# Optimization experiments

Measured on AMD Instinct MI355X. Metric: run time of the kernel, lower is better.

Reference implementation:

```python
import jax, jax.numpy as jnp
import numpy as np

N = 10000      # nodes
E = 160000     # edges (avg degree 16)
R = 4          # num_relations
H = 3          # heads
B = 100        # graphs in the batch
ED = 8         # edge_dim
NEG = 0.2      # leaky_relu negative slope (PyG default)

CONVS = [(768, 128), (256, 384), (256, 128), (256, 128)]  # (in, out) per RGATConv
LINS = [(128, 256), (384, 256), (128, 256), (128, 256)]


def setup_inputs() -> dict:
    key = jax.random.key(0)
    ks = iter(jax.random.split(key, 64))
    p = lambda shape: jax.random.normal(next(ks), shape, dtype=jnp.float32) * 0.05
    inp = {
        "x": jax.random.normal(next(ks), (N, 768), dtype=jnp.float32),
        "edge_index": jax.random.randint(next(ks), (2, E), 0, N),
        "edge_type": jax.random.randint(next(ks), (E,), 0, R),
        "edge_attr": jax.random.normal(next(ks), (E, ED), dtype=jnp.float32),
        "batch": jnp.repeat(jnp.arange(B, dtype=jnp.int32), N // B),  # sorted graph ids
    }
    for i, (cin, cout) in enumerate(CONVS, 1):
        ho = H * cout
        inp[f"W{i}"] = p((R, cin, ho))
        inp[f"q{i}"] = p((ho, H))
        inp[f"k{i}"] = p((ho, H))
        inp[f"le{i}"] = p((ED, ho))
        inp[f"e{i}"] = p((ho, H))
        inp[f"b{i}"] = jnp.zeros((cout,), jnp.float32)
    for i, (cin, cout) in enumerate(LINS, 1):
        inp[f"lw{i}"] = p((cin, cout))
        inp[f"lb{i}"] = jnp.zeros((cout,), jnp.float32)
    return inp


def _segment_softmax(a, index, n):
    # softmax of per-edge scores a (E, H) over destination-node segments
    amax = jax.ops.segment_max(a, index, num_segments=n)
    amax = jnp.where(jnp.isfinite(amax), amax, 0.0)
    ex = jnp.exp(a - amax[index])
    s = jax.ops.segment_sum(ex, index, num_segments=n)
    return ex / jnp.maximum(s[index], 1e-16)


def _rgat(x, src, dst, etype, eattr, W, q, k, le, e, b, cout):
    n = x.shape[0]
    xW = jnp.einsum('ni,rio->nro', x, W)           # (N, R, H*O): per-relation transform
    qn = jnp.einsum('nro,oh->nrh', xW, q)          # node-level query scores
    kn = jnp.einsum('nro,oh->nrh', xW, k)          # node-level key scores
    qi = qn[dst, etype]                            # (E, H)
    kj = kn[src, etype]                            # (E, H)
    ae = (eattr @ le) @ e                          # (E, H) edge-feature scores
    alpha = jax.nn.leaky_relu(qi + kj + ae, NEG)
    alpha = _segment_softmax(alpha, dst, n)        # across-relation segment softmax
    outj = xW[src, etype].reshape(-1, H, cout)     # (E, H, O)
    msg = alpha[:, :, None] * outj
    aggr = jax.ops.segment_sum(msg, dst, num_segments=n)  # (N, H, O)
    return aggr.mean(axis=1) + b                   # concat=False -> mean over heads


def reference(x, edge_index, edge_type, edge_attr, batch,
              W1, q1, k1, le1, e1, b1, W2, q2, k2, le2, e2, b2,
              W3, q3, k3, le3, e3, b3, W4, q4, k4, le4, e4, b4,
              lw1, lb1, lw2, lb2, lw3, lb3, lw4, lb4):
    src, dst = edge_index[0], edge_index[1]
    convs = [(W1, q1, k1, le1, e1, b1), (W2, q2, k2, le2, e2, b2),
             (W3, q3, k3, le3, e3, b3), (W4, q4, k4, le4, e4, b4)]
    lins = [(lw1, lb1), (lw2, lb2), (lw3, lb3), (lw4, lb4)]
    h = x
    for (W, q, k, le, e, b), (lw, lb), (cin, cout) in zip(convs, lins, CONVS):
        h = _rgat(h, src, dst, edge_type, edge_attr, W, q, k, le, e, b, cout)
        h = h @ lw + lb
    # dropout is identity in eval; pick first node of each graph (hole node)
    hole_idx = jax.ops.segment_min(jnp.arange(h.shape[0]), batch, num_segments=B)
    return jax.nn.softmax(h[hole_idx], axis=1)     # (B, 256)
```

## Files before the change

### kernel.cpp

```cpp
#include <hip/hip_runtime.h>

typedef unsigned int uint;
typedef unsigned short ushort;
typedef __attribute__((ext_vector_type(8))) short bf16x8;
typedef __attribute__((ext_vector_type(4))) float f32x4;

#define GLD_LDS(g, l) __builtin_amdgcn_global_load_lds( \
    (const __attribute__((address_space(1))) void*)(g), \
    (__attribute__((address_space(3))) void*)(l), 16, 0, 0)

__device__ __forceinline__ ushort f2bf(float f) {
    uint u = __builtin_bit_cast(uint, f);
    u += 0x7fffu + ((u >> 16) & 1u);
    return (ushort)(u >> 16);
}
__device__ __forceinline__ float bf2f(ushort s) {
    uint u = ((uint)s) << 16;
    return __builtin_bit_cast(float, u);
}
__device__ __forceinline__ void wave_sync() {
    asm volatile("s_waitcnt lgkmcnt(0)" ::: "memory");
}
__device__ __forceinline__ float wave_max(float v) {
#pragma unroll
    for (int d = 32; d >= 1; d >>= 1) v = fmaxf(v, __shfl_xor(v, d));
    return v;
}
__device__ __forceinline__ float wave_sum(float v) {
#pragma unroll
    for (int d = 32; d >= 1; d >>= 1) v += __shfl_xor(v, d);
    return v;
}

__global__ void deg_hole_kernel(const int* __restrict__ dst, int* __restrict__ cnt,
                                const int* __restrict__ bat, int* __restrict__ hole,
                                int E, int N) {
    int e = blockIdx.x * 256 + threadIdx.x;
    if (e < E) atomicAdd(&cnt[dst[e]], 1);
    if (e < N) atomicMin(&hole[bat[e]], e);
}

__global__ void scan_kernel(const int* __restrict__ cnt, int* __restrict__ offs, int n) {
    __shared__ int part[1024];
    const int t = threadIdx.x;
    const int strip = (n + 1023) / 1024;
    int s = 0;
    for (int i = 0; i < strip; ++i) {
        int idx = t * strip + i;
        if (idx < n) s += cnt[idx];
    }
    part[t] = s;
    __syncthreads();
    for (int d = 1; d < 1024; d <<= 1) {
        int v = (t >= d) ? part[t - d] : 0;
        __syncthreads();
        part[t] += v;
        __syncthreads();
    }
    int run = (t == 0) ? 0 : part[t - 1];
    for (int i = 0; i < strip; ++i) {
        int idx = t * strip + i;
        if (idx < n) { offs[idx] = run; run += cnt[idx]; }
    }
    if (t == 1023) offs[n] = part[1023];
}

__global__ void fill_kernel(const int* __restrict__ dst, const int* __restrict__ offs,
                            int* __restrict__ cur, int* __restrict__ csr, int E) {
    int e = blockIdx.x * 256 + threadIdx.x;
    if (e < E) {
        int d = dst[e];
        int p = offs[d] + atomicAdd(&cur[d], 1);
        csr[p] = e;
    }
}

struct PrepSArgs {
    const float *W0, *W1, *W2, *W3, *q0, *q1, *q2, *q3, *k0, *k1, *k2, *k3;
    float *Wqk0, *Wqk1, *Wqk2, *Wqk3;
    const float *le0, *le1, *le2, *le3, *e0, *e1, *e2, *e3;
    float* g;
    const float *b2, *lw2l, *lb2;
    float* bf2;
};

__device__ __forceinline__ void wqk_body(const float* W, const float* q, const float* k,
                                         float* Wqk, int cin, int ho, int i, int lane) {
    int c = i >> 2, r = i & 3;
    const float* wrow = W + ((long)r * cin + c) * ho;
    float sq0 = 0.f, sq1 = 0.f, sq2 = 0.f, sk0 = 0.f, sk1 = 0.f, sk2 = 0.f;
    for (int o = lane; o < ho; o += 64) {
        float w = wrow[o];
        sq0 += w * q[(long)o * 3 + 0];
        sq1 += w * q[(long)o * 3 + 1];
        sq2 += w * q[(long)o * 3 + 2];
        sk0 += w * k[(long)o * 3 + 0];
        sk1 += w * k[(long)o * 3 + 1];
        sk2 += w * k[(long)o * 3 + 2];
    }
    sq0 = wave_sum(sq0); sq1 = wave_sum(sq1); sq2 = wave_sum(sq2);
    sk0 = wave_sum(sk0); sk1 = wave_sum(sk1); sk2 = wave_sum(sk2);
    if (lane == 0) {
        float* w6 = Wqk + (long)c * 24 + r * 6;
        w6[0] = sq0; w6[1] = sq1; w6[2] = sq2;
        w6[3] = sk0; w6[4] = sk1; w6[5] = sk2;
    }
}

__global__ __launch_bounds__(256)
void preps_kernel(PrepSArgs a) {
    const int wid = threadIdx.x >> 6, lane = threadIdx.x & 63;
    int w = blockIdx.x * 4 + wid;
    if (w < 96) {
        int l = w / 24, j = w % 24;
        int d = j / 3, h = j % 3;
        const float* le = (l == 0) ? a.le0 : (l == 1 ? a.le1 : (l == 2 ? a.le2 : a.le3));
        const float* e  = (l == 0) ? a.e0  : (l == 1 ? a.e1  : (l == 2 ? a.e2  : a.e3));
        int ho = (l == 1) ? 1152 : 384;
        float s = 0.f;
        for (int o = lane; o < ho; o += 64) s += le[(long)d * ho + o] * e[(long)o * 3 + h];
        s = wave_sum(s);
        if (lane == 0) a.g[l * 24 + j] = s;
        return;
    }
    w -= 96;
    if (w < 3072) { wqk_body(a.W0, a.q0, a.k0, a.Wqk0, 768, 384, w, lane); return; }
    w -= 3072;
    if (w < 1024) { wqk_body(a.W1, a.q1, a.k1, a.Wqk1, 256, 1152, w, lane); return; }
    w -= 1024;
    if (w < 1024) { wqk_body(a.W2, a.q2, a.k2, a.Wqk2, 256, 384, w, lane); return; }
    w -= 1024;
    if (w < 1024) { wqk_body(a.W3, a.q3, a.k3, a.Wqk3, 256, 384, w, lane); return; }
    w -= 1024;
    if (w < 256) {
        float s = 0.f;
        for (int o = lane; o < 384; o += 64) s += a.b2[o] * a.lw2l[(long)o * 256 + w];
        s = wave_sum(s);
        if (lane == 0) a.bf2[w] = s + a.lb2[w];
    }
}

struct PrepWArgs {
    const float *x, *W0, *W2, *W3, *lw0, *lw1, *lw2, *lw3, *W1;
    ushort *hbf, *Wt0, *Wt2, *Wt3, *lwT0, *lwT1, *lwT2, *lwT3, *A2;
    const float* Wqk0;
};

__device__ __forceinline__ void trW_body(const float* W, ushort* Wt, int cin, int ho, long idx) {
    long ncol = idx / cin;
    int c = (int)(idx % cin);
    int r = (int)(ncol / ho);
    int o = (int)(ncol % ho);
    Wt[idx] = f2bf(W[((long)r * cin + c) * ho + o]);
}
__device__ __forceinline__ void trLw_body(const float* lw, ushort* lwT, int cout_in, long idx) {
    int o = (int)(idx / cout_in);
    int c = (int)(idx % cout_in);
    lwT[idx] = f2bf(lw[(long)c * 256 + o]);
}

__global__ __launch_bounds__(256)
void prepw_kernel(PrepWArgs a, int nbCast, long nCast) {
    int b = blockIdx.x;
    const int t = threadIdx.x;
    if (b < nbCast) {
        long i = ((long)b * 256 + t) * 4;
        if (i + 4 <= nCast) {
            float4 v = *(const float4*)(a.x + i);
            ushort4 o4 = { f2bf(v.x), f2bf(v.y), f2bf(v.z), f2bf(v.w) };
            *(ushort4*)(a.hbf + i) = o4;
        }
        return;
    }
    b -= nbCast;
    if (b < 4608) { trW_body(a.W0, a.Wt0, 768, 384, (long)b * 256 + t); return; }
    b -= 4608;
    if (b < 1536) { trW_body(a.W2, a.Wt2, 256, 384, (long)b * 256 + t); return; }
    b -= 1536;
    if (b < 1536) { trW_body(a.W3, a.Wt3, 256, 384, (long)b * 256 + t); return; }
    b -= 1536;
    if (b < 128)  { trLw_body(a.lw0, a.lwT0, 128, (long)b * 256 + t); return; }
    b -= 128;
    if (b < 384)  { trLw_body(a.lw1, a.lwT1, 384, (long)b * 256 + t); return; }
    b -= 384;
    if (b < 128)  { trLw_body(a.lw2, a.lwT2, 128, (long)b * 256 + t); return; }
    b -= 128;
    if (b < 128)  { trLw_body(a.lw3, a.lwT3, 128, (long)b * 256 + t); return; }
    b -= 128;
    if (b < 1728) {
        long idx = (long)b * 256 + t;
        int j = (int)(idx / 384), o = (int)(idx % 384);
        int h = j >> 10, rc = j & 1023;
        int r = rc >> 8, c = rc & 255;
        a.A2[idx] = f2bf(a.W1[((long)(r * 256 + c)) * 1152 + h * 384 + o] * (1.f / 3.f));
        return;
    }
    b -= 1728;
    if (b < 72) {
        long idx = (long)b * 256 + t;
        int j = (int)(idx / 768), c = (int)(idx % 768);
        a.Wt0[(long)(1536 + j) * 768 + c] = f2bf(a.Wqk0[(long)c * 24 + j]);
        return;
    }
    b -= 72;
    a.Wt0[(long)1560 * 768 + (long)b * 256 + t] = 0;
}

__global__ __launch_bounds__(256)
void prep2_kernel(const float* __restrict__ ea, const float* __restrict__ g,
                  float* __restrict__ aeb, int E, int nbAe,
                  const float* __restrict__ lw0, const float* __restrict__ Wqk1,
                  const float* __restrict__ lb0, ushort* __restrict__ lwT0, float* __restrict__ qb1,
                  const float* __restrict__ lw2, const float* __restrict__ Wqk3,
                  const float* __restrict__ lb2, ushort* __restrict__ lwT2, float* __restrict__ qb3) {
    int b = blockIdx.x;
    const int t = threadIdx.x;
    if (b < nbAe) {
        int e = b * 256 + t;
        if (e >= E) return;
        float a[8];
#pragma unroll
        for (int d = 0; d < 8; ++d) a[d] = ea[(long)e * 8 + d];
#pragma unroll
        for (int l = 0; l < 4; ++l) {
#pragma unroll
            for (int h = 0; h < 3; ++h) {
                float s = 0.f;
#pragma unroll
                for (int d = 0; d < 8; ++d) s += a[d] * g[l * 24 + d * 3 + h];
                aeb[((size_t)l * E + e) * 3 + h] = s;
            }
        }
        return;
    }
    b -= nbAe;
    const int wid = t >> 6, lane = t & 63;
    if (b < 768) {
        int w = b * 4 + wid;
        int c = w / 24, j = w % 24;
        float s = 0.f;
        for (int o = lane; o < 256; o += 64) s += lw0[(long)c * 256 + o] * Wqk1[(long)o * 24 + j];
        s = wave_sum(s);
        if (lane == 0) lwT0[(256 + j) * 128 + c] = f2bf(s);
        return;
    }
    b -= 768;
    if (b < 768) {
        int w = b * 4 + wid;
        int c = w / 24, j = w % 24;
        float s = 0.f;
        for (int o = lane; o < 256; o += 64) s += lw2[(long)c * 256 + o] * Wqk3[(long)o * 24 + j];
        s = wave_sum(s);
        if (lane == 0) lwT2[(256 + j) * 128 + c] = f2bf(s);
        return;
    }
    b -= 768;
    if (b < 6) {
        int w = b * 4 + wid;
        if (w < 24) {
            float s = 0.f;
            for (int o = lane; o < 256; o += 64) s += lb0[o] * Wqk1[(long)o * 24 + w];
            s = wave_sum(s);
            if (lane == 0) qb1[w] = s;
        }
        return;
    }
    b -= 6;
    if (b < 6) {
        int w = b * 4 + wid;
        if (w < 24) {
            float s = 0.f;
            for (int o = lane; o < 256; o += 64) s += lb2[o] * Wqk3[(long)o * 24 + w];
            s = wave_sum(s);
            if (lane == 0) qb3[w] = s;
        }
        return;
    }
    b -= 6;
    if (b < 52) { lwT0[280 * 128 + b * 256 + t] = 0; return; }
    b -= 52;
    lwT2[280 * 128 + b * 256 + t] = 0;
}

template<int OUT_BF16, int DUAL, int PARTIAL, int QK>
__global__ __launch_bounds__(256, 5)
void gemm_bf16(const ushort* __restrict__ A, const ushort* __restrict__ Bt,
               void* __restrict__ Cp, ushort* __restrict__ C2,
               const float* __restrict__ bias,
               int M, int K, int ldc, int nbn, int nwg, int nbase, int Ks,
               float* __restrict__ qkn, const float* __restrict__ qb, int qkcol) {
    __shared__ ushort lA[2][128 * 32];
    __shared__ ushort lB[2][128 * 32];
    const int t = threadIdx.x;
    const int lane = t & 63;
    const int wid = t >> 6;

    int b = blockIdx.x;
    int q8 = nwg >> 3, r8 = nwg & 7;
    int xcd = b & 7, loc = b >> 3;
    int tt = (xcd < r8 ? xcd * (q8 + 1) : r8 * (q8 + 1) + (xcd - r8) * q8) + loc;
    const int slice = tt / nbase;
    const int tile = tt % nbase;
    const int kbase = slice * Ks;
    const int bm = (tile / nbn) * 128;
    const int bn = (tile % nbn) * 128;

    const int wr = (wid >> 1) * 64;
    const int wc = (wid & 1) * 64;

    f32x4 acc[4][4];
#pragma unroll
    for (int m = 0; m < 4; ++m)
#pragma unroll
        for (int nn = 0; nn < 4; ++nn) acc[m][nn] = (f32x4){0.f, 0.f, 0.f, 0.f};

    const int sr = t >> 2;
    const int sk = (((t & 3) ^ ((t >> 3) & 3)) * 8);
    long ar0 = bm + sr;      if (ar0 > M - 1) ar0 = M - 1;
    long ar1 = bm + sr + 64; if (ar1 > M - 1) ar1 = M - 1;
    const ushort* gA0 = A + ar0 * K + sk + kbase;
    const ushort* gA1 = A + ar1 * K + sk + kbase;
    const ushort* gB0 = Bt + (long)(bn + sr) * K + sk + kbase;
    const ushort* gB1 = Bt + (long)(bn + sr + 64) * K + sk + kbase;

    const int frow = lane & 15;
    const int pc8 = (((lane >> 4) ^ ((lane >> 1) & 3)) * 8);

    GLD_LDS(gA0, &lA[0][t * 8]);
    GLD_LDS(gA1, &lA[0][t * 8 + 64 * 32]);
    GLD_LDS(gB0, &lB[0][t * 8]);
    GLD_LDS(gB1, &lB[0][t * 8 + 64 * 32]);
    __syncthreads();

    int cur = 0;
    for (int k0 = 0; k0 < Ks; k0 += 32) {
        if (k0 + 32 < Ks) {
            int nb = cur ^ 1, kn = k0 + 32;
            GLD_LDS(gA0 + kn, &lA[nb][t * 8]);
            GLD_LDS(gA1 + kn, &lA[nb][t * 8 + 64 * 32]);
            GLD_LDS(gB0 + kn, &lB[nb][t * 8]);
            GLD_LDS(gB1 + kn, &lB[nb][t * 8 + 64 * 32]);
        }
        bf16x8 af[4], bff[4];
#pragma unroll
        for (int m = 0; m < 4; ++m)
            af[m] = *(const bf16x8*)&lA[cur][(wr + m * 16 + frow) * 32 + pc8];
#pragma unroll
        for (int nn = 0; nn < 4; ++nn)
            bff[nn] = *(const bf16x8*)&lB[cur][(wc + nn * 16 + frow) * 32 + pc8];
#pragma unroll
        for (int m = 0; m < 4; ++m)
#pragma unroll
            for (int nn = 0; nn < 4; ++nn)
                acc[m][nn] = __builtin_amdgcn_mfma_f32_16x16x32_bf16(af[m], bff[nn], acc[m][nn], 0, 0, 0);
        __syncthreads();
        cur ^= 1;
    }

    const int crow = (lane >> 4) * 4;
    const int ccol = lane & 15;
#pragma unroll
    for (int m = 0; m < 4; ++m) {
#pragma unroll
        for (int nn = 0; nn < 4; ++nn) {
            int col = bn + wc + nn * 16 + ccol;
#pragma unroll
            for (int r = 0; r < 4; ++r) {
                int row = bm + wr + m * 16 + crow + r;
                if (row < M) {
                    float v = acc[m][nn][r];
                    if (QK && col >= qkcol) {
                        int qc = col - qkcol;
                        if (qc < 24) qkn[(long)row * 24 + qc] = v + (qb ? qb[qc] : 0.f);
                    } else {
                        if (!PARTIAL && bias) v += bias[col];
                        if (PARTIAL) {
                            ((float*)Cp)[(size_t)slice * M * ldc + (long)row * ldc + col] = v;
                        } else {
                            if (OUT_BF16) ((ushort*)Cp)[(long)row * ldc + col] = f2bf(v);
                            else          ((float*)Cp)[(long)row * ldc + col] = v;
                            if (DUAL)     C2[(long)row * ldc + col] = f2bf(v);
                        }
                    }
                }
            }
        }
    }
}

__global__ __launch_bounds__(256)
void reduce3qk_kernel(const float* __restrict__ P, const float* __restrict__ bf2,
                      const float* __restrict__ Wqk2,
                      float* __restrict__ outf, ushort* __restrict__ outb,
                      float* __restrict__ qkn, int M) {
    const int wid = threadIdx.x >> 6, lane = threadIdx.x & 63;
    const int n = blockIdx.x * 4 + wid;
    if (n >= M) return;
    long off = (long)n * 256 + lane * 4;
    const long stride = (long)M * 256;
    float4 a = *(const float4*)(P + off);
    float4 b = *(const float4*)(P + stride + off);
    float4 c = *(const float4*)(P + 2 * stride + off);
    float4 bs = *(const float4*)(bf2 + lane * 4);
    float rr[4] = { a.x + b.x + c.x + bs.x, a.y + b.y + c.y + bs.y,
                    a.z + b.z + c.z + bs.z, a.w + b.w + c.w + bs.w };
    float4 r4 = { rr[0], rr[1], rr[2], rr[3] };
    *(float4*)(outf + off) = r4;
    ushort4 o4 = { f2bf(rr[0]), f2bf(rr[1]), f2bf(rr[2]), f2bf(rr[3]) };
    *(ushort4*)(outb + off) = o4;
    float acc[24];
#pragma unroll
    for (int j = 0; j < 24; ++j) acc[j] = 0.f;
#pragma unroll
    for (int i = 0; i < 4; ++i) {
        const float* wr = Wqk2 + (long)(lane * 4 + i) * 24;
        float hv = rr[i];
#pragma unroll
        for (int j = 0; j < 24; ++j) acc[j] += hv * wr[j];
    }
#pragma unroll
    for (int j = 0; j < 24; ++j) {
        float v = wave_sum(acc[j]);
        if (lane == 0) qkn[(long)n * 24 + j] = v;
    }
}

__global__ __launch_bounds__(256)
void attn_kernel(const float* __restrict__ qkn, const ushort* __restrict__ xW,
                 const float* __restrict__ ae, const int* __restrict__ offs,
                 const int* __restrict__ csr, const int* __restrict__ srcv,
                 const int* __restrict__ etv, const float* __restrict__ bias,
                 ushort* __restrict__ out, int N) {
    __shared__ float4 pk_sh[4][64];
    __shared__ float red[4][384];
    const int wid = threadIdx.x >> 6, lane = threadIdx.x & 63;
    const int n = blockIdx.x * 4 + wid;
    if (n >= N) return;
    const int e0 = offs[n];
    const int deg = offs[n + 1] - e0;
    const float* qd = qkn + (long)n * 24;

    float m0 = -1e30f, m1 = -1e30f, m2 = -1e30f;
    for (int base = 0; base < deg; base += 64) {
        int idx = base + lane;
        if (idx < deg) {
            int eid = csr[e0 + idx];
            int s_ = srcv[eid], t_ = etv[eid];
            const float* qs = qkn + (long)s_ * 24 + t_ * 6;
            const float* a3 = ae + (long)eid * 3;
            float v0 = qd[t_ * 6 + 0] + qs[3] + a3[0];
            float v1 = qd[t_ * 6 + 1] + qs[4] + a3[1];
            float v2 = qd[t_ * 6 + 2] + qs[5] + a3[2];
            v0 = v0 > 0.f ? v0 : 0.2f * v0;
            v1 = v1 > 0.f ? v1 : 0.2f * v1;
            v2 = v2 > 0.f ? v2 : 0.2f * v2;
            m0 = fmaxf(m0, v0); m1 = fmaxf(m1, v1); m2 = fmaxf(m2, v2);
        }
    }
    m0 = wave_max(m0); m1 = wave_max(m1); m2 = wave_max(m2);

    float acc[6] = {0.f, 0.f, 0.f, 0.f, 0.f, 0.f};
    float ps0 = 0.f, ps1 = 0.f, ps2 = 0.f;

    for (int base = 0; base < deg; base += 64) {
        int cnt2 = deg - base; if (cnt2 > 64) cnt2 = 64;
        if (lane < cnt2) {
            int eid = csr[e0 + base + lane];
            int s_ = srcv[eid], t_ = etv[eid];
            const float* qs = qkn + (long)s_ * 24 + t_ * 6;
            const float* a3 = ae + (long)eid * 3;
            float v0 = qd[t_ * 6 + 0] + qs[3] + a3[0];
            float v1 = qd[t_ * 6 + 1] + qs[4] + a3[1];
            float v2 = qd[t_ * 6 + 2] + qs[5] + a3[2];
            v0 = v0 > 0.f ? v0 : 0.2f * v0;
            v1 = v1 > 0.f ? v1 : 0.2f * v1;
            v2 = v2 > 0.f ? v2 : 0.2f * v2;
            float p0 = __expf(v0 - m0), p1 = __expf(v1 - m1), p2 = __expf(v2 - m2);
            pk_sh[wid][lane] = make_float4(p0, p1, p2, __int_as_float((s_ << 2) | t_));
            ps0 += p0; ps1 += p1; ps2 += p2;
        }
        wave_sync();
        float4 pk0 = {0,0,0,0}, pk1 = {0,0,0,0}, pk2 = {0,0,0,0}, pk3 = {0,0,0,0};
        uint a0 = 0, b0 = 0, c0 = 0, a1 = 0, b1 = 0, c1 = 0;
        uint a2 = 0, b2 = 0, c2 = 0, a3 = 0, b3 = 0, c3 = 0;
#define LDE(S, J) { pk##S = pk_sh[wid][J]; \
    const uint* xr = (const uint*)(xW + (long)__float_as_int(pk##S.w) * 384); \
    a##S = xr[lane]; b##S = xr[lane + 64]; c##S = xr[lane + 128]; }
#define ACCE(S) { \
    acc[0] += pk##S.x * bf2f((ushort)(a##S & 0xffffu)); \
    acc[1] += pk##S.x * bf2f((ushort)(a##S >> 16)); \
    acc[2] += pk##S.y * bf2f((ushort)(b##S & 0xffffu)); \
    acc[3] += pk##S.y * bf2f((ushort)(b##S >> 16)); \
    acc[4] += pk##S.z * bf2f((ushort)(c##S & 0xffffu)); \
    acc[5] += pk##S.z * bf2f((ushort)(c##S >> 16)); }
        if (0 < cnt2) LDE(0, 0);
        if (1 < cnt2) LDE(1, 1);
        if (2 < cnt2) LDE(2, 2);
        if (3 < cnt2) LDE(3, 3);
        for (int j = 0; j < cnt2; j += 4) {
            { ACCE(0); if (j + 4 < cnt2) LDE(0, j + 4); }
            if (j + 1 < cnt2) { ACCE(1); if (j + 5 < cnt2) LDE(1, j + 5); }
            if (j + 2 < cnt2) { ACCE(2); if (j + 6 < cnt2) LDE(2, j + 6); }
            if (j + 3 < cnt2) { ACCE(3); if (j + 7 < cnt2) LDE(3, j + 7); }
        }
#undef LDE
#undef ACCE
        wave_sync();
    }
    ps0 = wave_sum(ps0); ps1 = wave_sum(ps1); ps2 = wave_sum(ps2);
    float i0 = 1.f / fmaxf(ps0, 1e-16f);
    float i1 = 1.f / fmaxf(ps1, 1e-16f);
    float i2 = 1.f / fmaxf(ps2, 1e-16f);
    red[wid][2 * lane]           = acc[0] * i0;
    red[wid][2 * lane + 1]       = acc[1] * i0;
    red[wid][128 + 2 * lane]     = acc[2] * i1;
    red[wid][128 + 2 * lane + 1] = acc[3] * i1;
    red[wid][256 + 2 * lane]     = acc[4] * i2;
    red[wid][256 + 2 * lane + 1] = acc[5] * i2;
    wave_sync();
    for (int o = lane; o < 128; o += 64) {
        float v = (red[wid][o] + red[wid][128 + o] + red[wid][256 + o]) * (1.f / 3.f) + bias[o];
        out[(long)n * 128 + o] = f2bf(v);
    }
}

__global__ __launch_bounds__(256)
void attn2_kernel(const float* __restrict__ qkn, const ushort* __restrict__ hbf,
                  const float* __restrict__ ae, const int* __restrict__ offs,
                  const int* __restrict__ csr, const int* __restrict__ srcv,
                  const int* __restrict__ etv, ushort* __restrict__ Z, int N) {
    __shared__ float4 pk_sh[4][64];
    const int wid = threadIdx.x >> 6, lane = threadIdx.x & 63;
    const int n = blockIdx.x * 4 + wid;
    if (n >= N) return;
    const int e0 = offs[n];
    const int deg = offs[n + 1] - e0;
    const float* qd = qkn + (long)n * 24;

    float m0 = -1e30f, m1 = -1e30f, m2 = -1e30f;
    for (int base = 0; base < deg; base += 64) {
        int idx = base + lane;
        if (idx < deg) {
            int eid = csr[e0 + idx];
            int s_ = srcv[eid], t_ = etv[eid];
            const float* qs = qkn + (long)s_ * 24 + t_ * 6;
            const float* a3 = ae + (long)eid * 3;
            float v0 = qd[t_ * 6 + 0] + qs[3] + a3[0];
            float v1 = qd[t_ * 6 + 1] + qs[4] + a3[1];
            float v2 = qd[t_ * 6 + 2] + qs[5] + a3[2];
            v0 = v0 > 0.f ? v0 : 0.2f * v0;
            v1 = v1 > 0.f ? v1 : 0.2f * v1;
            v2 = v2 > 0.f ? v2 : 0.2f * v2;
            m0 = fmaxf(m0, v0); m1 = fmaxf(m1, v1); m2 = fmaxf(m2, v2);
        }
    }
    m0 = wave_max(m0); m1 = wave_max(m1); m2 = wave_max(m2);

    float acc[48];
#pragma unroll
    for (int i = 0; i < 48; ++i) acc[i] = 0.f;
    float ps0 = 0.f, ps1 = 0.f, ps2 = 0.f;

    for (int base = 0; base < deg; base += 64) {
        int cnt2 = deg - base; if (cnt2 > 64) cnt2 = 64;
        if (lane < cnt2) {
            int eid = csr[e0 + base + lane];
            int s_ = srcv[eid], t_ = etv[eid];
            const float* qs = qkn + (long)s_ * 24 + t_ * 6;
            const float* a3 = ae + (long)eid * 3;
            float v0 = qd[t_ * 6 + 0] + qs[3] + a3[0];
            float v1 = qd[t_ * 6 + 1] + qs[4] + a3[1];
            float v2 = qd[t_ * 6 + 2] + qs[5] + a3[2];
            v0 = v0 > 0.f ? v0 : 0.2f * v0;
            v1 = v1 > 0.f ? v1 : 0.2f * v1;
            v2 = v2 > 0.f ? v2 : 0.2f * v2;
            float p0 = __expf(v0 - m0), p1 = __expf(v1 - m1), p2 = __expf(v2 - m2);
            pk_sh[wid][lane] = make_float4(p0, p1, p2, __int_as_float((s_ << 2) | t_));
            ps0 += p0; ps1 += p1; ps2 += p2;
        }
        wave_sync();
        float4 pk0 = {0,0,0,0}, pk1 = {0,0,0,0}, pk2 = {0,0,0,0}, pk3 = {0,0,0,0};
        uint2 v0_ = {0,0}, v1_ = {0,0}, v2_ = {0,0}, v3_ = {0,0};
#define LDE2(S, J) { pk##S = pk_sh[wid][J]; \
    v##S##_ = *(const uint2*)(hbf + ((long)(__float_as_int(pk##S.w) >> 2)) * 256 + lane * 4); }
#define UPDR(R) { \
    acc[(R)*4+0] += px * x0; acc[(R)*4+1] += px * x1; acc[(R)*4+2] += px * x2; acc[(R)*4+3] += px * x3; \
    acc[16+(R)*4+0] += py * x0; acc[16+(R)*4+1] += py * x1; acc[16+(R)*4+2] += py * x2; acc[16+(R)*4+3] += py * x3; \
    acc[32+(R)*4+0] += pz * x0; acc[32+(R)*4+1] += pz * x1; acc[32+(R)*4+2] += pz * x2; acc[32+(R)*4+3] += pz * x3; }
#define ACC2(S) { int r_ = __float_as_int(pk##S.w) & 3; \
    float x0 = bf2f((ushort)(v##S##_.x & 0xffffu)), x1 = bf2f((ushort)(v##S##_.x >> 16)); \
    float x2 = bf2f((ushort)(v##S##_.y & 0xffffu)), x3 = bf2f((ushort)(v##S##_.y >> 16)); \
    float px = pk##S.x, py = pk##S.y, pz = pk##S.z; \
    if (r_ == 0) UPDR(0) else if (r_ == 1) UPDR(1) else if (r_ == 2) UPDR(2) else UPDR(3) }
        if (0 < cnt2) LDE2(0, 0);
        if (1 < cnt2) LDE2(1, 1);
        if (2 < cnt2) LDE2(2, 2);
        if (3 < cnt2) LDE2(3, 3);
        for (int j = 0; j < cnt2; j += 4) {
            { ACC2(0); if (j + 4 < cnt2) LDE2(0, j + 4); }
            if (j + 1 < cnt2) { ACC2(1); if (j + 5 < cnt2) LDE2(1, j + 5); }
            if (j + 2 < cnt2) { ACC2(2); if (j + 6 < cnt2) LDE2(2, j + 6); }
            if (j + 3 < cnt2) { ACC2(3); if (j + 7 < cnt2) LDE2(3, j + 7); }
        }
#undef LDE2
#undef UPDR
#undef ACC2
        wave_sync();
    }
    ps0 = wave_sum(ps0); ps1 = wave_sum(ps1); ps2 = wave_sum(ps2);
    float inv0 = 1.f / fmaxf(ps0, 1e-16f);
    float inv1 = 1.f / fmaxf(ps1, 1e-16f);
    float inv2 = 1.f / fmaxf(ps2, 1e-16f);
    ushort* zr = Z + (long)n * 3072 + lane * 4;
#pragma unroll
    for (int h = 0; h < 3; ++h) {
        float iv = (h == 0) ? inv0 : (h == 1 ? inv1 : inv2);
#pragma unroll
        for (int r = 0; r < 4; ++r) {
            const float* a4 = acc + h * 16 + r * 4;
            ushort4 o4 = { f2bf(a4[0] * iv), f2bf(a4[1] * iv),
                           f2bf(a4[2] * iv), f2bf(a4[3] * iv) };
            *(ushort4*)(zr + h * 1024 + r * 256) = o4;
        }
    }
}

__global__ void softmax_kernel(const float* __restrict__ h, const int* __restrict__ hole,
                               float* __restrict__ out, int B) {
    int b = blockIdx.x;
    int t = threadIdx.x;
    int lane = t & 63, wid = t >> 6;
    __shared__ float sm[4];
    __shared__ float ss[4];
    int row = hole[b];
    float v = h[(long)row * 256 + t];
    float m = v;
#pragma unroll
    for (int d = 32; d >= 1; d >>= 1) m = fmaxf(m, __shfl_xor(m, d));
    if (lane == 0) sm[wid] = m;
    __syncthreads();
    m = fmaxf(fmaxf(sm[0], sm[1]), fmaxf(sm[2], sm[3]));
    float ex = __expf(v - m);
    float s = ex;
#pragma unroll
    for (int d = 32; d >= 1; d >>= 1) s += __shfl_xor(s, d);
    if (lane == 0) ss[wid] = s;
    __syncthreads();
    s = ss[0] + ss[1] + ss[2] + ss[3];
    out[(long)b * 256 + t] = ex / s;
}

extern "C" void kernel_launch(void* const* d_in, const int* in_sizes, int n_in,
                              void* d_out, int out_size, void* d_ws, size_t ws_size,
                              hipStream_t stream) {
    const float* x   = (const float*)d_in[0];
    const int*   ei  = (const int*)d_in[1];
    const int*   ety = (const int*)d_in[2];
    const float* ea  = (const float*)d_in[3];
    const int*   bat = (const int*)d_in[4];

    const int N = in_sizes[0] / 768;
    const int E = in_sizes[2];
    const int B = out_size / 256;

    static const int CIN[4]  = {768, 256, 256, 256};
    static const int COUT[4] = {128, 384, 128, 128};
    static const int NCC[4]  = {1536, 4608, 1536, 1536};

    const float *Wp[4], *qp[4], *kp[4], *lep[4], *ep[4], *bp[4], *lwp[4], *lbp[4];
    for (int l = 0; l < 4; ++l) {
        Wp[l]  = (const float*)d_in[5 + 6 * l];
        qp[l]  = (const float*)d_in[6 + 6 * l];
        kp[l]  = (const float*)d_in[7 + 6 * l];
        lep[l] = (const float*)d_in[8 + 6 * l];
        ep[l]  = (const float*)d_in[9 + 6 * l];
        bp[l]  = (const float*)d_in[10 + 6 * l];
        lwp[l] = (const float*)d_in[29 + 2 * l];
        lbp[l] = (const float*)d_in[30 + 2 * l];
    }

    char* ws = (char*)d_ws;
    size_t pos = 0;
    auto carve = [&](size_t bytes) -> char* {
        char* r = ws + pos;
        pos += (bytes + 255) & ~(size_t)255;
        return r;
    };
    ushort *Wt[4], *lwT[4];
    float* Wqk[4];
    for (int l = 0; l < 4; ++l) {
        size_t cols = (l == 0) ? 1664 : (size_t)NCC[l];
        Wt[l] = (ushort*)carve(l == 1 ? 0 : (size_t)2 * cols * CIN[l]);
    }
    for (int l = 0; l < 4; ++l) lwT[l] = (ushort*)carve((size_t)2 * 384 * COUT[l]);
    for (int l = 0; l < 4; ++l) Wqk[l] = (float*)carve((size_t)4 * 24 * CIN[l]);
    float*  gbuf  = (float*)carve(4 * 24 * 4);
    float*  aeb   = (float*)carve((size_t)4 * E * 3 * 4);
    float*  qkn   = (float*)carve((size_t)N * 24 * 4);
    float*  qb1   = (float*)carve(24 * 4);
    float*  qb3   = (float*)carve(24 * 4);
    ushort* hbf   = (ushort*)carve((size_t)N * 768 * 2);
    ushort* xWb   = (ushort*)carve((size_t)N * 1536 * 2);
    ushort* Zb    = (ushort*)carve((size_t)N * 3072 * 2);
    ushort* A2    = (ushort*)carve((size_t)3072 * 384 * 2);
    ushort* W2T   = (ushort*)carve((size_t)256 * 3072 * 2);
    float*  bf2   = (float*)carve(256 * 4);
    ushort* convbf= (ushort*)carve((size_t)N * 384 * 2);
    float*  hbuf  = (float*)carve((size_t)N * 256 * 4);
    int* cnt  = (int*)carve((size_t)N * 4);
    int* cur  = (int*)carve((size_t)N * 4);
    int* offs = (int*)carve((size_t)(N + 1) * 4);
    int* csr  = (int*)carve((size_t)E * 4);
    int* hole = (int*)carve((size_t)B * 4);

    hipMemsetAsync(cnt, 0, (size_t)((char*)cur - (char*)cnt) + (size_t)N * 4, stream);
    hipMemsetAsync(hole, 0x7f, (size_t)B * 4, stream);

    const int* dst = ei + E;
    int nbEH = ((E > N ? E : N) + 255) / 256;
    deg_hole_kernel<<<nbEH, 256, 0, stream>>>(dst, cnt, bat, hole, E, N);
    scan_kernel<<<1, 1024, 0, stream>>>(cnt, offs, N);
    fill_kernel<<<(E + 255) / 256, 256, 0, stream>>>(dst, offs, cur, csr, E);

    PrepSArgs psa = { Wp[0], Wp[1], Wp[2], Wp[3], qp[0], qp[1], qp[2], qp[3],
                      kp[0], kp[1], kp[2], kp[3], Wqk[0], Wqk[1], Wqk[2], Wqk[3],
                      lep[0], lep[1], lep[2], lep[3], ep[0], ep[1], ep[2], ep[3],
                      gbuf, bp[1], lwp[1], lbp[1], bf2 };
    preps_kernel<<<(6496 + 3) / 4, 256, 0, stream>>>(psa);

    long nCast = (long)N * 768;
    int nbCast = (int)((nCast / 4 + 255) / 256);
    PrepWArgs pw = { x, Wp[0], Wp[2], Wp[3], lwp[0], lwp[1], lwp[2], lwp[3], Wp[1],
                     hbf, Wt[0], Wt[2], Wt[3], lwT[0], lwT[1], lwT[2], lwT[3], A2, Wqk[0] };
    prepw_kernel<<<nbCast + 13056 + 72 + 312, 256, 0, stream>>>(pw, nbCast, nCast);

    int nbAe = (E + 255) / 256;
    prep2_kernel<<<nbAe + 1652, 256, 0, stream>>>(ea, gbuf, aeb, E, nbAe,
                                                  lwp[0], Wqk[1], lbp[0], lwT[0], qb1,
                                                  lwp[2], Wqk[3], lbp[2], lwT[2], qb3);

    gemm_bf16<1, 0, 0, 0><<<48, 256, 0, stream>>>(lwT[1], A2, (void*)W2T, nullptr, nullptr,
                                                  256, 384, 3072, 24, 48, 48, 384,
                                                  nullptr, nullptr, 0);

    const int nbm = (N + 127) / 128;
    for (int l = 0; l < 4; ++l) {
        if (l == 1) {
            attn2_kernel<<<(N + 3) / 4, 256, 0, stream>>>(qkn, hbf, aeb + (size_t)l * E * 3,
                                                          offs, csr, ei, ety, Zb, N);
            int nbase = nbm * 2, nwgS = nbase * 3;
            gemm_bf16<0, 0, 1, 0><<<nwgS, 256, 0, stream>>>(Zb, W2T, (void*)xWb, nullptr, nullptr,
                                                            N, 3072, 256, 2, nwgS, nbase, 1024,
                                                            nullptr, nullptr, 0);
            reduce3qk_kernel<<<(N + 3) / 4, 256, 0, stream>>>((const float*)xWb, bf2, Wqk[2],
                                                              hbuf, hbf, qkn, N);
        } else {
            if (l == 0) {
                int nbn1 = 13, nwg1 = nbm * nbn1;
                gemm_bf16<1, 0, 0, 1><<<nwg1, 256, 0, stream>>>(hbf, Wt[0], (void*)xWb, nullptr,
                                                                nullptr, N, 768, 1536, nbn1, nwg1,
                                                                nwg1, 768, qkn, nullptr, 1536);
            } else {
                int nbn1 = NCC[l] / 128, nwg1 = nbm * nbn1;
                gemm_bf16<1, 0, 0, 0><<<nwg1, 256, 0, stream>>>(hbf, Wt[l], (void*)xWb, nullptr,
                                                                nullptr, N, CIN[l], NCC[l], nbn1,
                                                                nwg1, nwg1, CIN[l],
                                                                nullptr, nullptr, 0);
            }
            attn_kernel<<<(N + 3) / 4, 256, 0, stream>>>(qkn, xWb, aeb + (size_t)l * E * 3,
                                                         offs, csr, ei, ety, bp[l], convbf, N);
            if (l == 3) {
                int nwg2 = nbm * 2;
                gemm_bf16<0, 0, 0, 0><<<nwg2, 256, 0, stream>>>(convbf, lwT[3], (void*)hbuf, nullptr,
                                                                lbp[3], N, 128, 256, 2, nwg2, nwg2, 128,
                                                                nullptr, nullptr, 0);
            } else {
                float* qbp = (l == 0) ? qb1 : qb3;
                int nwg2 = nbm * 3;
                gemm_bf16<0, 1, 0, 1><<<nwg2, 256, 0, stream>>>(convbf, lwT[l], (void*)hbuf, hbf,
                                                                lbp[l], N, 128, 256, 3, nwg2, nwg2, 128,
                                                                qkn, qbp, 256);
            }
        }
    }
    softmax_kernel<<<B, 256, 0, stream>>>(hbuf, hole, (float*)d_out, B);
}
```

Before: 461.1 us.

## Merge prep kernels and compute layer-0 q/k scores in a separate wave-per-node kernel

Layer 0 no longer appends 24 q/k columns (padded to 1664) to the first GEMM's weight. A dedicated qk0 kernel instead computes the q/k node scores from the bf16 input with one wave per node. The layer-0 GEMM drops from 13 to 12 column tiles and loses its QK epilogue. The separate prep2 kernel is folded into prepw_kernel to save a launch. The new qk0 kernel rereads the whole 768-wide bf16 input and does scalar FMA work, which may cost more than the extra GEMM tile it replaces.

```diff
diff --git a/kernel.cpp b/kernel.cpp
--- a/kernel.cpp
+++ b/kernel.cpp
@@ -143,7 +143,10 @@
 struct PrepWArgs {
     const float *x, *W0, *W2, *W3, *lw0, *lw1, *lw2, *lw3, *W1;
     ushort *hbf, *Wt0, *Wt2, *Wt3, *lwT0, *lwT1, *lwT2, *lwT3, *A2;
-    const float* Wqk0;
+    const float *ea, *g;
+    float* aeb;
+    const float *Wqk1, *Wqk3, *lb0, *lb2;
+    float *qb1, *qb3;
 };
 
 __device__ __forceinline__ void trW_body(const float* W, ushort* Wt, int cin, int ho, long idx) {
@@ -160,7 +163,7 @@
 }
 
 __global__ __launch_bounds__(256)
-void prepw_kernel(PrepWArgs a, int nbCast, long nCast) {
+void prepw_kernel(PrepWArgs a, int nbCast, long nCast, int E, int nbAe) {
     int b = blockIdx.x;
     const int t = threadIdx.x;
     if (b < nbCast) {
@@ -196,39 +199,20 @@
         return;
     }
     b -= 1728;
-    if (b < 72) {
-        long idx = (long)b * 256 + t;
-        int j = (int)(idx / 768), c = (int)(idx % 768);
-        a.Wt0[(long)(1536 + j) * 768 + c] = f2bf(a.Wqk0[(long)c * 24 + j]);
-        return;
-    }
-    b -= 72;
-    a.Wt0[(long)1560 * 768 + (long)b * 256 + t] = 0;
-}
-
-__global__ __launch_bounds__(256)
-void prep2_kernel(const float* __restrict__ ea, const float* __restrict__ g,
-                  float* __restrict__ aeb, int E, int nbAe,
-                  const float* __restrict__ lw0, const float* __restrict__ Wqk1,
-                  const float* __restrict__ lb0, ushort* __restrict__ lwT0, float* __restrict__ qb1,
-                  const float* __restrict__ lw2, const float* __restrict__ Wqk3,
-                  const float* __restrict__ lb2, ushort* __restrict__ lwT2, float* __restrict__ qb3) {
-    int b = blockIdx.x;
-    const int t = threadIdx.x;
     if (b < nbAe) {
         int e = b * 256 + t;
         if (e >= E) return;
-        float a[8];
-#pragma unroll
-        for (int d = 0; d < 8; ++d) a[d] = ea[(long)e * 8 + d];
+        float av[8];
+#pragma unroll
+        for (int d = 0; d < 8; ++d) av[d] = a.ea[(long)e * 8 + d];
 #pragma unroll
         for (int l = 0; l < 4; ++l) {
 #pragma unroll
             for (int h = 0; h < 3; ++h) {
                 float s = 0.f;
 #pragma unroll
-                for (int d = 0; d < 8; ++d) s += a[d] * g[l * 24 + d * 3 + h];
-                aeb[((size_t)l * E + e) * 3 + h] = s;
+                for (int d = 0; d < 8; ++d) s += av[d] * a.g[l * 24 + d * 3 + h];
+                a.aeb[((size_t)l * E + e) * 3 + h] = s;
             }
         }
         return;
@@ -239,9 +223,9 @@
         int w = b * 4 + wid;
         int c = w / 24, j = w % 24;
         float s = 0.f;
-        for (int o = lane; o < 256; o += 64) s += lw0[(long)c * 256 + o] * Wqk1[(long)o * 24 + j];
+        for (int o = lane; o < 256; o += 64) s += a.lw0[(long)c * 256 + o] * a.Wqk1[(long)o * 24 + j];
         s = wave_sum(s);
-        if (lane == 0) lwT0[(256 + j) * 128 + c] = f2bf(s);
+        if (lane == 0) a.lwT0[(256 + j) * 128 + c] = f2bf(s);
         return;
     }
     b -= 768;
@@ -249,9 +233,9 @@
         int w = b * 4 + wid;
         int c = w / 24, j = w % 24;
         float s = 0.f;
-        for (int o = lane; o < 256; o += 64) s += lw2[(long)c * 256 + o] * Wqk3[(long)o * 24 + j];
+        for (int o = lane; o < 256; o += 64) s += a.lw2[(long)c * 256 + o] * a.Wqk3[(long)o * 24 + j];
         s = wave_sum(s);
-        if (lane == 0) lwT2[(256 + j) * 128 + c] = f2bf(s);
+        if (lane == 0) a.lwT2[(256 + j) * 128 + c] = f2bf(s);
         return;
     }
     b -= 768;
@@ -259,9 +243,9 @@
         int w = b * 4 + wid;
         if (w < 24) {
             float s = 0.f;
-            for (int o = lane; o < 256; o += 64) s += lb0[o] * Wqk1[(long)o * 24 + w];
+            for (int o = lane; o < 256; o += 64) s += a.lb0[o] * a.Wqk1[(long)o * 24 + w];
             s = wave_sum(s);
-            if (lane == 0) qb1[w] = s;
+            if (lane == 0) a.qb1[w] = s;
         }
         return;
     }
@@ -270,16 +254,44 @@
         int w = b * 4 + wid;
         if (w < 24) {
             float s = 0.f;
-            for (int o = lane; o < 256; o += 64) s += lb2[o] * Wqk3[(long)o * 24 + w];
+            for (int o = lane; o < 256; o += 64) s += a.lb2[o] * a.Wqk3[(long)o * 24 + w];
             s = wave_sum(s);
-            if (lane == 0) qb3[w] = s;
+            if (lane == 0) a.qb3[w] = s;
         }
         return;
     }
     b -= 6;
-    if (b < 52) { lwT0[280 * 128 + b * 256 + t] = 0; return; }
+    if (b < 52) { a.lwT0[280 * 128 + b * 256 + t] = 0; return; }
     b -= 52;
-    lwT2[280 * 128 + b * 256 + t] = 0;
+    a.lwT2[280 * 128 + b * 256 + t] = 0;
+}
+
+__global__ __launch_bounds__(256)
+void qk0_kernel(const ushort* __restrict__ hbf, const float* __restrict__ Wqk,
+                float* __restrict__ qkn, int N) {
+    const int wid = threadIdx.x >> 6, lane = threadIdx.x & 63;
+    const int n = blockIdx.x * 4 + wid;
+    if (n >= N) return;
+    float acc[24];
+#pragma unroll
+    for (int j = 0; j < 24; ++j) acc[j] = 0.f;
+    const ushort* hr = hbf + (long)n * 768;
+#pragma unroll
+    for (int k = 0; k < 3; ++k) {
+        int c0 = k * 256 + lane * 4;
+        uint2 v = *(const uint2*)(hr + c0);
+        float h0 = bf2f((ushort)(v.x & 0xffffu)), h1 = bf2f((ushort)(v.x >> 16));
+        float h2 = bf2f((ushort)(v.y & 0xffffu)), h3 = bf2f((ushort)(v.y >> 16));
+        const float* w0 = Wqk + (long)c0 * 24;
+#pragma unroll
+        for (int j = 0; j < 24; ++j)
+            acc[j] += h0 * w0[j] + h1 * w0[24 + j] + h2 * w0[48 + j] + h3 * w0[72 + j];
+    }
+#pragma unroll
+    for (int j = 0; j < 24; ++j) {
+        float v = wave_sum(acc[j]);
+        if (lane == 0) qkn[(long)n * 24 + j] = v;
+    }
 }
 
 template<int OUT_BF16, int DUAL, int PARTIAL, int QK>
@@ -688,10 +700,7 @@
     };
     ushort *Wt[4], *lwT[4];
     float* Wqk[4];
-    for (int l = 0; l < 4; ++l) {
-        size_t cols = (l == 0) ? 1664 : (size_t)NCC[l];
-        Wt[l] = (ushort*)carve(l == 1 ? 0 : (size_t)2 * cols * CIN[l]);
-    }
+    for (int l = 0; l < 4; ++l) Wt[l]  = (ushort*)carve(l == 1 ? 0 : (size_t)2 * NCC[l] * CIN[l]);
     for (int l = 0; l < 4; ++l) lwT[l] = (ushort*)carve((size_t)2 * 384 * COUT[l]);
     for (int l = 0; l < 4; ++l) Wqk[l] = (float*)carve((size_t)4 * 24 * CIN[l]);
     float*  gbuf  = (float*)carve(4 * 24 * 4);
@@ -730,18 +739,16 @@
 
     long nCast = (long)N * 768;
     int nbCast = (int)((nCast / 4 + 255) / 256);
+    int nbAe = (E + 255) / 256;
     PrepWArgs pw = { x, Wp[0], Wp[2], Wp[3], lwp[0], lwp[1], lwp[2], lwp[3], Wp[1],
-                     hbf, Wt[0], Wt[2], Wt[3], lwT[0], lwT[1], lwT[2], lwT[3], A2, Wqk[0] };
-    prepw_kernel<<<nbCast + 13056 + 72 + 312, 256, 0, stream>>>(pw, nbCast, nCast);
-
-    int nbAe = (E + 255) / 256;
-    prep2_kernel<<<nbAe + 1652, 256, 0, stream>>>(ea, gbuf, aeb, E, nbAe,
-                                                  lwp[0], Wqk[1], lbp[0], lwT[0], qb1,
-                                                  lwp[2], Wqk[3], lbp[2], lwT[2], qb3);
+                     hbf, Wt[0], Wt[2], Wt[3], lwT[0], lwT[1], lwT[2], lwT[3], A2,
+                     ea, gbuf, aeb, Wqk[1], Wqk[3], lbp[0], lbp[2], qb1, qb3 };
+    prepw_kernel<<<nbCast + 10176 + nbAe + 1652, 256, 0, stream>>>(pw, nbCast, nCast, E, nbAe);
 
     gemm_bf16<1, 0, 0, 0><<<48, 256, 0, stream>>>(lwT[1], A2, (void*)W2T, nullptr, nullptr,
                                                   256, 384, 3072, 24, 48, 48, 384,
                                                   nullptr, nullptr, 0);
+    qk0_kernel<<<(N + 3) / 4, 256, 0, stream>>>(hbf, Wqk[0], qkn, N);
 
     const int nbm = (N + 127) / 128;
     for (int l = 0; l < 4; ++l) {
@@ -755,18 +762,11 @@
             reduce3qk_kernel<<<(N + 3) / 4, 256, 0, stream>>>((const float*)xWb, bf2, Wqk[2],
                                                               hbuf, hbf, qkn, N);
         } else {
-            if (l == 0) {
-                int nbn1 = 13, nwg1 = nbm * nbn1;
-                gemm_bf16<1, 0, 0, 1><<<nwg1, 256, 0, stream>>>(hbf, Wt[0], (void*)xWb, nullptr,
-                                                                nullptr, N, 768, 1536, nbn1, nwg1,
-                                                                nwg1, 768, qkn, nullptr, 1536);
-            } else {
-                int nbn1 = NCC[l] / 128, nwg1 = nbm * nbn1;
-                gemm_bf16<1, 0, 0, 0><<<nwg1, 256, 0, stream>>>(hbf, Wt[l], (void*)xWb, nullptr,
-                                                                nullptr, N, CIN[l], NCC[l], nbn1,
-                                                                nwg1, nwg1, CIN[l],
-                                                                nullptr, nullptr, 0);
-            }
+            int nbn1 = NCC[l] / 128, nwg1 = nbm * nbn1;
+            gemm_bf16<1, 0, 0, 0><<<nwg1, 256, 0, stream>>>(hbf, Wt[l], (void*)xWb, nullptr,
+                                                            nullptr, N, CIN[l], NCC[l], nbn1,
+                                                            nwg1, nwg1, CIN[l],
+                                                            nullptr, nullptr, 0);
             attn_kernel<<<(N + 3) / 4, 256, 0, stream>>>(qkn, xWb, aeb + (size_t)l * E * 3,
                                                          offs, csr, ei, ety, bp[l], convbf, N);
             if (l == 3) {
```

Measured after the change: 589.2 us. 1.28x slower.
